# Performance work log

Measured on AMD Instinct MI355X. Metric: run time of the kernel, lower is better.

The kernel has to match this reference:

```python
import jax, jax.numpy as jnp
import numpy as np

B, L, N_SAMPLES = 16, 512, 512
N_REF = 1000


def _interp_row(xs, ys, q):
    # Linear interpolation with linear extrapolation at both ends,
    # matching torchinterp1d: ind = clamp(searchsorted(x, q) - 1, 0, n-2).
    n = xs.shape[0]
    i = jnp.clip(jnp.searchsorted(xs, q, side='left') - 1, 0, n - 2)
    x0 = xs[i]
    y0 = ys[i]
    slope = (ys[i + 1] - y0) / (xs[i + 1] - x0)
    return y0 + slope * (q - x0)


def interp1d(x, y, xq):
    # x, y: [b, l, n] (x sorted along last dim); xq: [b, l, m]
    b, l, n = x.shape
    m = xq.shape[-1]
    out = jax.vmap(_interp_row)(x.reshape(-1, n), y.reshape(-1, n), xq.reshape(-1, m))
    return out.reshape(b, l, m)


def emb(samples, ref):
    # samples: [b, l, n] circular samples in [0,1); ref: [N]
    b, l, n = samples.shape
    N = ref.shape[0]
    dt = samples.dtype

    xs = jnp.sort(samples, axis=-1)                                  # [b,l,n]
    ys = jnp.broadcast_to(jnp.arange(1, n + 1, dtype=dt) / n, (b, l, n))

    xnew = jnp.broadcast_to(jnp.linspace(-1.0, 2.0, 3 * N, dtype=dt), (b, l, 3 * N))
    int_x = jnp.floor(xnew)
    rest_x = xnew - int_x
    # circular ECDF extended to [-1, 2)
    ecdf_vals = int_x + interp1d(xs, ys, rest_x)                     # [b,l,3N]

    alpha = jnp.mean(samples, axis=-1, keepdims=True) - 0.5          # [b,l,1]
    x = jnp.broadcast_to(ref.astype(dt), (b, l, N))
    # inverse CDF (quantile) evaluated at x - alpha, minus identity map
    return interp1d(ecdf_vals, xnew, x - alpha) - x                  # [b,l,N]


def setup_inputs() -> dict:
    key = jax.random.key(0)
    k1, k2 = jax.random.split(key)
    x1 = jax.random.uniform(k1, (B, L, N_SAMPLES), dtype=jnp.float32)
    x2 = jax.random.uniform(k2, (B, L, N_SAMPLES), dtype=jnp.float32)
    ref = jnp.arange(N_REF, dtype=jnp.float32) / N_REF  # linspace(0,1,1001)[:-1]
    return {"x1": x1, "x2": x2, "ref": ref}


def reference(x1, x2, ref):
    e1 = emb(x1, ref)
    e2 = emb(x2, ref)
    d = jnp.abs(e2 - e1)
    circ = jnp.minimum(d, 1.0 - d)                                   # circular distance
    return jnp.sqrt(jnp.sum(circ * circ, axis=-1)).mean(-1)          # [b]
```

## Files before the change

### kernel.cpp

```cpp
#include <hip/hip_runtime.h>
#include <math.h>

#define NB 16
#define NL 512
#define NS 512
#define NE 3000
#define NR 1000
#define NROWS (NB * NL)
#define NBIN 512

__device__ __forceinline__ float fast_rcp(float x) { return __builtin_amdgcn_rcpf(x); }

__global__ __launch_bounds__(256) void lcot_row_kernel(
    const float* __restrict__ x1, const float* __restrict__ x2,
    const float* __restrict__ ref, float* __restrict__ row_out)
{
    __shared__ float    s_sorted[NS];
    __shared__ unsigned s_hist[NBIN];
    __shared__ unsigned s_prefix[NBIN + 1];
    __shared__ float    s_ecdf[NE];
    __shared__ float    s_alpA[4], s_alpB[4];
    __shared__ float    s_devf[4];
    __shared__ unsigned s_wredu[4];

    const int tid  = threadIdx.x;
    const int lane = tid & 63;
    const int wave = tid >> 6;
    const int row  = blockIdx.x;
    const float inv_n   = 1.0f / 512.0f;
    const float step    = (float)(3.0 / 2999.0);
    const float invstep = 2999.0f / 3.0f;

    const int j0 = tid * 4;
    float rj0 = 0.f, rj1 = 0.f, rj2 = 0.f, rj3 = 0.f;
    if (j0 < NR) {
        float4 r4 = ((const float4*)ref)[tid];
        rj0 = r4.x; rj1 = r4.y; rj2 = r4.z; rj3 = r4.w;
    }
    float e1r0 = 0.f, e1r1 = 0.f, e1r2 = 0.f, e1r3 = 0.f;

    const float* srcA = x1 + (size_t)row * NS;
    const float* srcB = x2 + (size_t)row * NS;
    float a0 = srcA[tid], a1 = srcA[tid + 256];
    float c0 = srcB[tid], c1 = srcB[tid + 256];

    float acc = 0.0f;

    for (int inp = 0; inp < 2; ++inp) {
        float v0 = (inp == 0) ? a0 : c0;
        float v1 = (inp == 0) ? a1 : c1;

        if (inp == 0) {
            s_hist[tid] = 0u;
            s_hist[tid + 256] = 0u;
            float sA = a0 + a1, sB = c0 + c1;
            #pragma unroll
            for (int o = 32; o > 0; o >>= 1) {
                sA += __shfl_down(sA, o, 64);
                sB += __shfl_down(sB, o, 64);
            }
            if (lane == 0) { s_alpA[wave] = sA; s_alpB[wave] = sB; }
            __syncthreads();
        }

        int b0 = min((int)(v0 * 512.0f), NBIN - 1);
        int b1 = min((int)(v1 * 512.0f), NBIN - 1);
        atomicAdd(&s_hist[b0], 1u);
        atomicAdd(&s_hist[b1], 1u);
        __syncthreads();

        const float* alp = (inp == 0) ? s_alpA : s_alpB;
        float alpha = (alp[0] + alp[1] + alp[2] + alp[3]) * inv_n - 0.5f;

        unsigned h0 = s_hist[2 * tid];
        unsigned h1 = s_hist[2 * tid + 1];
        unsigned ls = h0 + h1;
        unsigned sc0 = ls;
        #pragma unroll
        for (int o = 1; o < 64; o <<= 1) {
            unsigned t2 = __shfl_up(sc0, o, 64);
            if (lane >= o) sc0 += t2;
        }
        if (lane == 63) s_wredu[wave] = sc0;
        __syncthreads();
        unsigned wbase0 = 0;
        for (int w = 0; w < 4; ++w) if (w < wave) wbase0 += s_wredu[w];
        unsigned base = wbase0 + sc0 - ls;
        s_prefix[2 * tid]     = base;
        s_prefix[2 * tid + 1] = base + h0;
        s_hist[2 * tid]       = base;
        s_hist[2 * tid + 1]   = base + h0;
        if (tid == 255) s_prefix[NBIN] = (unsigned)NS;
        __syncthreads();

        unsigned p0 = atomicAdd(&s_hist[b0], 1u);
        s_sorted[p0] = v0;
        unsigned p1 = atomicAdd(&s_hist[b1], 1u);
        s_sorted[p1] = v1;
        float dv = fmaxf(fabsf((float)(p0 + 1) * inv_n - v0),
                         fabsf((float)(p1 + 1) * inv_n - v1));
        #pragma unroll
        for (int o = 32; o > 0; o >>= 1) dv = fmaxf(dv, __shfl_down(dv, o, 64));
        if (lane == 0) s_devf[wave] = dv;
        __syncthreads();

        for (int bb = tid; bb < NBIN; bb += 256) {
            int beg = (int)s_prefix[bb];
            int end = (int)s_prefix[bb + 1];
            for (int i2 = beg + 1; i2 < end; ++i2) {
                float key = s_sorted[i2];
                int jj = i2 - 1;
                while (jj >= beg && s_sorted[jj] > key) { s_sorted[jj + 1] = s_sorted[jj]; --jj; }
                s_sorted[jj + 1] = key;
            }
        }
        __syncthreads();

        float Dm = fmaxf(fmaxf(s_devf[0], s_devf[1]), fmaxf(s_devf[2], s_devf[3]));
        {
            float sa0 = s_sorted[0], sa1 = s_sorted[1];
            float sbA = s_sorted[510], sbB = s_sorted[511];
            float sl0 = inv_n * fast_rcp(sa1 - sa0);
            float slR = inv_n * fast_rcp(sbB - sbA);
            float lext = fabsf(inv_n - sl0 * sa0);
            float rext = fabsf(511.0f * inv_n + slR * (1.0f - sbA) - 1.0f);
            Dm = fmaxf(Dm, fmaxf(lext, rext));
        }
        float D = Dm + 0.0249f;

        float qlo = 0.0f - alpha;
        float qhi = 0.999f - alpha;
        int kmin = max(0,  (int)((qlo + 1.0f - D) * invstep) - 2);
        int kmax = min(NE, (int)((qhi + 1.0f + D) * invstep) + 3);

        {
            int W  = kmax - kmin;
            int k0 = kmin + ((tid * W) >> 8);
            int k1 = kmin + (((tid + 1) * W) >> 8);
            float fm = -100.0f;
            int pos = 0;
            int ci = -1;
            float cx0 = 0.f, cy0 = 0.f, cslope = 0.f;
            for (int k = k0; k < k1; ++k) {
                float xn  = -1.0f + (float)k * step;
                float fm2 = floorf(xn);
                float r   = xn - fm2;
                if (fm2 != fm) {
                    fm = fm2;
                    int bq  = min((int)(r * 512.0f), NBIN - 1);
                    pos     = (int)s_prefix[bq];
                    int be  = (int)s_prefix[bq + 1];
                    while (pos < be && s_sorted[pos] < r) ++pos;
                } else {
                    while (pos < NS && s_sorted[pos] < r) ++pos;
                }
                int i = min(max(pos - 1, 0), NS - 2);
                if (i != ci) {
                    ci = i;
                    cx0 = s_sorted[i];
                    cy0 = (float)(i + 1) * inv_n;
                    cslope = inv_n * fast_rcp(s_sorted[i + 1] - cx0);
                }
                s_ecdf[k] = fm + (cy0 + cslope * (r - cx0));
            }
        }
        if (inp == 0) { s_hist[tid] = 0u; s_hist[tid + 256] = 0u; }
        __syncthreads();

        if (j0 < NR) {
            float q = rj0 - alpha;
            int lo = kmin, hi = kmax;
            while (lo < hi) {
                int mid = (lo + hi) >> 1;
                if (s_ecdf[mid] < q) lo = mid + 1; else hi = mid;
            }
            int pos2 = lo;
            #pragma unroll
            for (int jj = 0; jj < 4; ++jj) {
                float rj = (jj == 0) ? rj0 : (jj == 1) ? rj1 : (jj == 2) ? rj2 : rj3;
                q = rj - alpha;
                if (jj > 0) while (pos2 < NE && s_ecdf[pos2] < q) ++pos2;
                int i = min(max(pos2 - 1, 0), NE - 2);
                float e0 = s_ecdf[i];
                float slope = step * fast_rcp(s_ecdf[i + 1] - e0);
                float xn0 = -1.0f + (float)i * step;
                float res = xn0 + slope * (q - e0);
                float embv = res - rj;
                if (inp == 0) {
                    if (jj == 0) e1r0 = embv;
                    else if (jj == 1) e1r1 = embv;
                    else if (jj == 2) e1r2 = embv;
                    else e1r3 = embv;
                } else {
                    float ev = (jj == 0) ? e1r0 : (jj == 1) ? e1r1 : (jj == 2) ? e1r2 : e1r3;
                    float d = fabsf(embv - ev);
                    float c = fminf(d, 1.0f - d);
                    acc = fmaf(c, c, acc);
                }
            }
        }
    }

    #pragma unroll
    for (int o = 32; o > 0; o >>= 1) acc += __shfl_down(acc, o, 64);
    if (lane == 0) s_devf[wave] = acc;
    __syncthreads();
    if (tid == 0) row_out[row] = sqrtf(s_devf[0] + s_devf[1] + s_devf[2] + s_devf[3]);
}

__global__ __launch_bounds__(256) void lcot_reduce_kernel(
    const float* __restrict__ row_vals, float* __restrict__ out)
{
    __shared__ float s_red[256];
    const int b = blockIdx.x;
    const int tid = threadIdx.x;
    float v = row_vals[b * NL + tid] + row_vals[b * NL + tid + 256];
    s_red[tid] = v;
    __syncthreads();
    for (int off = 128; off > 0; off >>= 1) {
        if (tid < off) s_red[tid] += s_red[tid + off];
        __syncthreads();
    }
    if (tid == 0) out[b] = s_red[0] * (1.0f / (float)NL);
}

extern "C" void kernel_launch(void* const* d_in, const int* in_sizes, int n_in,
                              void* d_out, int out_size, void* d_ws, size_t ws_size,
                              hipStream_t stream) {
    const float* x1  = (const float*)d_in[0];
    const float* x2  = (const float*)d_in[1];
    const float* ref = (const float*)d_in[2];
    float* out = (float*)d_out;
    float* row_vals = (float*)d_ws;

    lcot_row_kernel<<<NROWS, 256, 0, stream>>>(x1, x2, ref, row_vals);
    lcot_reduce_kernel<<<NB, 256, 0, stream>>>(row_vals, out);
}
```

Before: 106.2 us.

## Replace per-thread binary search with analytic ECDF inversion and fixed-chunk ECDF build

The inverse-CDF lookup no longer binary-searches the extended ECDF. It predicts the bracket position analytically from the sorted samples and then walks a few steps locally. References near the periodic seams (k≈1000, 2000), where the ECDF is non-monotone, are sent to a separate fallback binary-search pass, and first-input embeddings are stored in shared memory for that path. The ECDF build now gives each thread a fixed chunk of 5 entries plus a strided tail loop, instead of splitting the range proportionally. This adds code complexity and extra shared memory, and edge handling around the ambiguous ranges could diverge from the reference.

```diff
diff --git a/kernel.cpp b/kernel.cpp
--- a/kernel.cpp
+++ b/kernel.cpp
@@ -8,6 +8,7 @@
 #define NR 1000
 #define NROWS (NB * NL)
 #define NBIN 512
+#define CPT 5
 
 __device__ __forceinline__ float fast_rcp(float x) { return __builtin_amdgcn_rcpf(x); }
 
@@ -19,9 +20,11 @@
     __shared__ unsigned s_hist[NBIN];
     __shared__ unsigned s_prefix[NBIN + 1];
     __shared__ float    s_ecdf[NE];
+    __shared__ float4   s_e14[NR / 4];
     __shared__ float    s_alpA[4], s_alpB[4];
     __shared__ float    s_devf[4];
     __shared__ unsigned s_wredu[4];
+    float* s_e1 = (float*)s_e14;
 
     const int tid  = threadIdx.x;
     const int lane = tid & 63;
@@ -37,7 +40,6 @@
         float4 r4 = ((const float4*)ref)[tid];
         rj0 = r4.x; rj1 = r4.y; rj2 = r4.z; rj3 = r4.w;
     }
-    float e1r0 = 0.f, e1r1 = 0.f, e1r2 = 0.f, e1r3 = 0.f;
 
     const float* srcA = x1 + (size_t)row * NS;
     const float* srcB = x2 + (size_t)row * NS;
@@ -134,9 +136,8 @@
         int kmax = min(NE, (int)((qhi + 1.0f + D) * invstep) + 3);
 
         {
-            int W  = kmax - kmin;
-            int k0 = kmin + ((tid * W) >> 8);
-            int k1 = kmin + (((tid + 1) * W) >> 8);
+            int k0 = kmin + tid * CPT;
+            int k1 = min(k0 + CPT, kmax);
             float fm = -100.0f;
             int pos = 0;
             int ci = -1;
@@ -163,37 +164,122 @@
                 }
                 s_ecdf[k] = fm + (cy0 + cslope * (r - cx0));
             }
+            for (int k = kmin + 256 * CPT + tid; k < kmax; k += 256) {
+                float xn  = -1.0f + (float)k * step;
+                float fm2 = floorf(xn);
+                float r   = xn - fm2;
+                int bq  = min((int)(r * 512.0f), NBIN - 1);
+                int pp  = (int)s_prefix[bq];
+                int be  = (int)s_prefix[bq + 1];
+                while (pp < be && s_sorted[pp] < r) ++pp;
+                int i = min(max(pp - 1, 0), NS - 2);
+                float x0 = s_sorted[i];
+                float y0 = (float)(i + 1) * inv_n;
+                float sl = inv_n * fast_rcp(s_sorted[i + 1] - x0);
+                s_ecdf[k] = fm2 + (y0 + sl * (r - x0));
+            }
         }
         if (inp == 0) { s_hist[tid] = 0u; s_hist[tid + 256] = 0u; }
         __syncthreads();
 
+        const float INF = 3.0e38f;
+        bool in0 = (kmin <= 999)  && (1000 < kmax);
+        bool in1 = (kmin <= 1999) && (2000 < kmax);
+        float t0a = in0 ? s_ecdf[999]  : 0.f;
+        float t0b = in0 ? s_ecdf[1000] : 0.f;
+        float t1a = in1 ? s_ecdf[1999] : 0.f;
+        float t1b = in1 ? s_ecdf[2000] : 0.f;
+        float rt0 = in0 ? t0b : ((kmin > 999)  ? -INF : INF);
+        float rt1 = in1 ? t1b : ((kmin > 1999) ? -INF : INF);
+        int jA0 = 1, jA1 = 0, jB0 = 1, jB1 = 0;
+        if (in0 && t0b < t0a) {
+            jA0 = max((int)floorf((t0b + alpha) * 1000.0f) + 1, 0);
+            jA1 = min((int)floorf((t0a + alpha) * 1000.0f), NR - 1);
+        }
+        if (in1 && t1b < t1a) {
+            jB0 = max((int)floorf((t1b + alpha) * 1000.0f) + 1, 0);
+            jB1 = min((int)floorf((t1a + alpha) * 1000.0f), NR - 1);
+        }
+
         if (j0 < NR) {
-            float q = rj0 - alpha;
-            int lo = kmin, hi = kmax;
-            while (lo < hi) {
-                int mid = (lo + hi) >> 1;
-                if (s_ecdf[mid] < q) lo = mid + 1; else hi = mid;
-            }
-            int pos2 = lo;
+            float4 e1v4 = make_float4(0.f, 0.f, 0.f, 0.f);
+            if (inp == 1) e1v4 = ((const float4*)s_e1)[tid];
+            float o0 = 0.f, o1 = 0.f, o2 = 0.f, o3 = 0.f;
+            bool am0 = false, am1 = false, am2 = false, am3 = false;
+            int  k = kmin;
+            bool have = false;
             #pragma unroll
             for (int jj = 0; jj < 4; ++jj) {
+                int  j  = j0 + jj;
                 float rj = (jj == 0) ? rj0 : (jj == 1) ? rj1 : (jj == 2) ? rj2 : rj3;
-                q = rj - alpha;
-                if (jj > 0) while (pos2 < NE && s_ecdf[pos2] < q) ++pos2;
-                int i = min(max(pos2 - 1, 0), NE - 2);
+                bool amb = (j >= jA0 && j <= jA1) || (j >= jB0 && j <= jB1);
+                if (jj == 0) am0 = amb; else if (jj == 1) am1 = amb;
+                else if (jj == 2) am2 = amb; else am3 = amb;
+                if (!amb) {
+                    float q = rj - alpha;
+                    if (!have) {
+                        int m = (q > rt0) + (q > rt1) - 1;
+                        float u = q - (float)m;
+                        int istar = min(max((int)ceilf(u * 512.0f) - 2, 0), NS - 2);
+                        float xa = s_sorted[istar];
+                        float xb = s_sorted[istar + 1];
+                        float rstar = fmaf(u - (float)(istar + 1) * inv_n,
+                                           512.0f * (xb - xa), xa);
+                        float xstar = (float)m + rstar;
+                        k = min(max((int)ceilf((xstar + 1.0f) * invstep) - 1, kmin), kmax - 2);
+                        have = true;
+                    }
+                    while (k < kmax - 2 && s_ecdf[k + 1] < q) ++k;
+                    while (k > kmin && s_ecdf[k] >= q) --k;
+                    float e0  = s_ecdf[k];
+                    float e1c = s_ecdf[k + 1];
+                    float slope = step * fast_rcp(e1c - e0);
+                    float xn0 = -1.0f + (float)k * step;
+                    float embv = xn0 + slope * (q - e0) - rj;
+                    if (inp == 0) {
+                        if (jj == 0) o0 = embv; else if (jj == 1) o1 = embv;
+                        else if (jj == 2) o2 = embv; else o3 = embv;
+                    } else {
+                        float ev = (jj == 0) ? e1v4.x : (jj == 1) ? e1v4.y
+                                 : (jj == 2) ? e1v4.z : e1v4.w;
+                        float d = fabsf(embv - ev);
+                        float c = fminf(d, 1.0f - d);
+                        acc = fmaf(c, c, acc);
+                    }
+                }
+            }
+            if (inp == 0) {
+                if (!(am0 | am1 | am2 | am3)) {
+                    ((float4*)s_e1)[tid] = make_float4(o0, o1, o2, o3);
+                } else {
+                    if (!am0) s_e1[j0]     = o0;
+                    if (!am1) s_e1[j0 + 1] = o1;
+                    if (!am2) s_e1[j0 + 2] = o2;
+                    if (!am3) s_e1[j0 + 3] = o3;
+                }
+            }
+        }
+
+        for (int pass = 0; pass < 2; ++pass) {
+            int lo0 = pass ? jB0 : jA0;
+            int hi0 = pass ? jB1 : jA1;
+            for (int j = lo0 + tid; j <= hi0; j += 256) {
+                float rj = ref[j];
+                float q  = rj - alpha;
+                int lo = kmin, hi = kmax;
+                while (lo < hi) {
+                    int mid = (lo + hi) >> 1;
+                    if (s_ecdf[mid] < q) lo = mid + 1; else hi = mid;
+                }
+                int i = min(max(lo - 1, 0), NE - 2);
                 float e0 = s_ecdf[i];
                 float slope = step * fast_rcp(s_ecdf[i + 1] - e0);
                 float xn0 = -1.0f + (float)i * step;
-                float res = xn0 + slope * (q - e0);
-                float embv = res - rj;
+                float embv = xn0 + slope * (q - e0) - rj;
                 if (inp == 0) {
-                    if (jj == 0) e1r0 = embv;
-                    else if (jj == 1) e1r1 = embv;
-                    else if (jj == 2) e1r2 = embv;
-                    else e1r3 = embv;
+                    s_e1[j] = embv;
                 } else {
-                    float ev = (jj == 0) ? e1r0 : (jj == 1) ? e1r1 : (jj == 2) ? e1r2 : e1r3;
-                    float d = fabsf(embv - ev);
+                    float d = fabsf(embv - s_e1[j]);
                     float c = fminf(d, 1.0f - d);
                     acc = fmaf(c, c, acc);
                 }
```

After: 123.4 us. +16.2%, slower.

## Replace quantile binary search with analytic ECDF inversion and local walk

Applied to the files above, without the earlier changes.

The inverse-CDF lookup now predicts the ecdf index analytically. It inverts the piecewise-linear sample ECDF through the sorted samples, then walks locally, and keeps a binary search only for queries near the integer seams where the ECDF may be non-monotone. The ECDF construction loop also caches the next sorted sample in a register to avoid rereading shared memory. This is meant to remove about a dozen dependent LDS reads per thread from the binary search, at the cost of more branching and added correctness reasoning around the seams.

```diff
diff --git a/kernel.cpp b/kernel.cpp
--- a/kernel.cpp
+++ b/kernel.cpp
@@ -141,6 +141,7 @@
             int pos = 0;
             int ci = -1;
             float cx0 = 0.f, cy0 = 0.f, cslope = 0.f;
+            float snext = 0.f;
             for (int k = k0; k < k1; ++k) {
                 float xn  = -1.0f + (float)k * step;
                 float fm2 = floorf(xn);
@@ -151,8 +152,12 @@
                     pos     = (int)s_prefix[bq];
                     int be  = (int)s_prefix[bq + 1];
                     while (pos < be && s_sorted[pos] < r) ++pos;
+                    snext = (pos < NS) ? s_sorted[pos] : 2.0f;
                 } else {
-                    while (pos < NS && s_sorted[pos] < r) ++pos;
+                    while (pos < NS && snext < r) {
+                        ++pos;
+                        snext = (pos < NS) ? s_sorted[pos] : 2.0f;
+                    }
                 }
                 int i = min(max(pos - 1, 0), NS - 2);
                 if (i != ci) {
@@ -167,25 +172,59 @@
         if (inp == 0) { s_hist[tid] = 0u; s_hist[tid + 256] = 0u; }
         __syncthreads();
 
+        const float INF = 3.0e38f;
+        bool in0 = (kmin <= 999)  && (1000 < kmax);
+        bool in1 = (kmin <= 1999) && (2000 < kmax);
+        float t0a = in0 ? s_ecdf[999]  : 0.f;
+        float t0b = in0 ? s_ecdf[1000] : 0.f;
+        float t1a = in1 ? s_ecdf[1999] : 0.f;
+        float t1b = in1 ? s_ecdf[2000] : 0.f;
+        float rt0 = in0 ? t0b : ((kmin > 999)  ? -INF : INF);
+        float rt1 = in1 ? t1b : ((kmin > 1999) ? -INF : INF);
+
         if (j0 < NR) {
-            float q = rj0 - alpha;
-            int lo = kmin, hi = kmax;
-            while (lo < hi) {
-                int mid = (lo + hi) >> 1;
-                if (s_ecdf[mid] < q) lo = mid + 1; else hi = mid;
-            }
-            int pos2 = lo;
+            int  k = kmin;
+            bool have = false;
             #pragma unroll
             for (int jj = 0; jj < 4; ++jj) {
                 float rj = (jj == 0) ? rj0 : (jj == 1) ? rj1 : (jj == 2) ? rj2 : rj3;
-                q = rj - alpha;
-                if (jj > 0) while (pos2 < NE && s_ecdf[pos2] < q) ++pos2;
-                int i = min(max(pos2 - 1, 0), NE - 2);
-                float e0 = s_ecdf[i];
-                float slope = step * fast_rcp(s_ecdf[i + 1] - e0);
-                float xn0 = -1.0f + (float)i * step;
-                float res = xn0 + slope * (q - e0);
-                float embv = res - rj;
+                float q = rj - alpha;
+                float embv;
+                bool amb = (q > t0b && q <= t0a) || (q > t1b && q <= t1a);
+                if (amb) {
+                    int lo = kmin, hi = kmax;
+                    while (lo < hi) {
+                        int mid = (lo + hi) >> 1;
+                        if (s_ecdf[mid] < q) lo = mid + 1; else hi = mid;
+                    }
+                    int i = min(max(lo - 1, 0), NE - 2);
+                    float e0 = s_ecdf[i];
+                    float slope = step * fast_rcp(s_ecdf[i + 1] - e0);
+                    float xn0 = -1.0f + (float)i * step;
+                    float res = xn0 + slope * (q - e0);
+                    embv = res - rj;
+                } else {
+                    if (!have) {
+                        int m = (q > rt0) + (q > rt1) - 1;
+                        float u = q - (float)m;
+                        int istar = min(max((int)ceilf(u * 512.0f) - 2, 0), NS - 2);
+                        float xa = s_sorted[istar];
+                        float xb = s_sorted[istar + 1];
+                        float rstar = fmaf(u - (float)(istar + 1) * inv_n,
+                                           512.0f * (xb - xa), xa);
+                        float xstar = (float)m + rstar;
+                        k = min(max((int)ceilf((xstar + 1.0f) * invstep) - 1, kmin), kmax - 2);
+                        have = true;
+                    }
+                    while (k < kmax - 2 && s_ecdf[k + 1] < q) ++k;
+                    while (k > kmin && s_ecdf[k] >= q) --k;
+                    float e0  = s_ecdf[k];
+                    float e1c = s_ecdf[k + 1];
+                    float slope = step * fast_rcp(e1c - e0);
+                    float xn0 = -1.0f + (float)k * step;
+                    float res = xn0 + slope * (q - e0);
+                    embv = res - rj;
+                }
                 if (inp == 0) {
                     if (jj == 0) e1r0 = embv;
                     else if (jj == 1) e1r1 = embv;
```

New measurement: 118.7 us. +11.8%, slower.
